# Kernel tuning notes

Hardware: AMD Instinct MI355X
Metric: run time of the kernel (lower is better)

The kernel has to match this reference:

```python
import jax, jax.numpy as jnp
import numpy as np

EPS = 1e-12  # torch F.normalize default eps (clamp_min)

def _l2norm(v, axis):
    n = jnp.sqrt(jnp.sum(v * v, axis=axis, keepdims=True))
    return v / jnp.maximum(n, EPS)

def setup_inputs() -> dict:
    key = jax.random.key(0)
    k1, k2, k3 = jax.random.split(key, 3)
    N, D, H, W, K = 64, 128, 64, 64, 32
    x = jax.random.normal(k1, (N, D, H, W), dtype=jnp.float32)
    conv_w = jax.random.normal(k2, (K, D), dtype=jnp.float32)  # 1x1 conv weight, no bias
    centroids = jax.random.uniform(k3, (K, D), dtype=jnp.float32)
    return {"x": x, "conv_w": conv_w, "centroids": centroids}

def reference(x, conv_w, centroids):
    N, D, H, W = x.shape
    K = conv_w.shape[0]
    # descriptor-wise L2 normalization over channel dim
    x = _l2norm(x, axis=1)
    xf = x.reshape(N, D, H * W)                      # [N, D, P]
    # 1x1 conv == per-pixel linear: [K,D] @ [N,D,P] -> [N,K,P]
    logits = jnp.einsum('kd,ndp->nkp', conv_w, xf)
    soft_assign = jax.nn.softmax(logits, axis=1)     # softmax over clusters
    # vlad[n,k,d] = sum_p a[n,k,p]*(x[n,d,p] - c[k,d])
    #            = (a @ x^T)[n,k,d] - (sum_p a)[n,k] * c[k,d]
    agg = jnp.einsum('nkp,ndp->nkd', soft_assign, xf)
    asum = jnp.sum(soft_assign, axis=2)              # [N, K]
    vlad = agg - asum[:, :, None] * centroids[None]  # [N, K, D]
    vlad = _l2norm(vlad, axis=2)                     # intra-normalization
    vlad = vlad.reshape(N, K * D)
    vlad = _l2norm(vlad, axis=1)                     # global L2 norm
    return vlad
```

## Files before the change

kernel.cpp:

```cpp
#include <hip/hip_runtime.h>
#include <math.h>

#define N_IMG 64
#define D_CH  128
#define P_PIX 4096
#define K_CL  32
#define S_SPL 8
#define P_BLK (P_PIX / S_SPL)
#define TP    32
#define N_TILE (P_BLK / TP)

typedef __attribute__((ext_vector_type(8))) short bf16x8;
typedef __attribute__((ext_vector_type(4))) float f32x4;

#define MFMA(a, b, c) __builtin_amdgcn_mfma_f32_16x16x32_bf16(a, b, c, 0, 0, 0)

#define BAR() do {                                            \
    asm volatile("s_waitcnt lgkmcnt(0)" ::: "memory");        \
    __builtin_amdgcn_s_barrier();                             \
} while (0)

static __device__ __forceinline__ ushort f2bf_rne(float f) {
    unsigned u = __float_as_uint(f);
    unsigned r = u + 0x7fffu + ((u >> 16) & 1u);
    return (ushort)(r >> 16);
}
static __device__ __forceinline__ ushort4 rne4(float a, float b, float c, float d) {
    ushort4 h;
    h.x = f2bf_rne(a); h.y = f2bf_rne(b); h.z = f2bf_rne(c); h.w = f2bf_rne(d);
    return h;
}

static __device__ __forceinline__ void split4t(float a, float b, float c, float d,
                                               ushort4 &h, ushort4 &l) {
    unsigned ua = __float_as_uint(a), ub = __float_as_uint(b);
    unsigned uc = __float_as_uint(c), ud = __float_as_uint(d);
    h.x = (ushort)(ua >> 16); h.y = (ushort)(ub >> 16);
    h.z = (ushort)(uc >> 16); h.w = (ushort)(ud >> 16);
    float ra = a - __uint_as_float(ua & 0xffff0000u);
    float rb = b - __uint_as_float(ub & 0xffff0000u);
    float rc = c - __uint_as_float(uc & 0xffff0000u);
    float rd = d - __uint_as_float(ud & 0xffff0000u);
    l.x = (ushort)(__float_as_uint(ra) >> 16);
    l.y = (ushort)(__float_as_uint(rb) >> 16);
    l.z = (ushort)(__float_as_uint(rc) >> 16);
    l.w = (ushort)(__float_as_uint(rd) >> 16);
}

#define STAGE_AND_PREFETCH(tt) do {                                          \
    const int cc_ = (tt) & 1;                                                \
    _Pragma("unroll")                                                        \
    for (int it = 0; it < 4; ++it) {                                         \
        int d_ = it * 32 + (tid >> 3);                                       \
        *(ushort4*)&xDh[cc_][d_ * 40 + 4 * (tid & 7)] =                      \
            rne4(xv[it].x, xv[it].y, xv[it].z, xv[it].w);                    \
    }                                                                        \
    float sq_ = 0.f;                                                         \
    _Pragma("unroll")                                                        \
    for (int c_ = 0; c_ < 4; ++c_) {                                         \
        *(ushort4*)&xTh[pT * 136 + dbase + 4 * c_] =                         \
            rne4(tv[4*c_+0], tv[4*c_+1], tv[4*c_+2], tv[4*c_+3]);            \
        sq_ += tv[4*c_+0]*tv[4*c_+0] + tv[4*c_+1]*tv[4*c_+1]                 \
             + tv[4*c_+2]*tv[4*c_+2] + tv[4*c_+3]*tv[4*c_+3];                \
    }                                                                        \
    sq_ += __shfl_xor(sq_, 32);                                              \
    if (l < 32) pbuf[wid][pT] = sq_;                                         \
    if ((tt) + 1 < N_TILE) {                                                 \
        const float* xt2_ = xin + ((tt) + 1) * TP;                           \
        _Pragma("unroll")                                                    \
        for (int it = 0; it < 4; ++it) {                                     \
            int d_ = it * 32 + (tid >> 3);                                   \
            xv[it] = *(const float4*)(xt2_ + d_ * P_PIX + 4 * (tid & 7));    \
        }                                                                    \
        _Pragma("unroll")                                                    \
        for (int j_ = 0; j_ < 16; ++j_)                                      \
            tv[j_] = xt2_[(size_t)(dbase + j_) * P_PIX + pT];                \
    }                                                                        \
} while (0)

__global__ __launch_bounds__(256)
void netvlad_main(const float* __restrict__ x, const float* __restrict__ w,
                  float* __restrict__ aggp, float* __restrict__ asump)
{
    __shared__ __align__(16) ushort xTh[32 * 136];
    __shared__ __align__(16) ushort xDh[2][128 * 40];
    __shared__ __align__(16) ushort aph[2][32 * 40];
    __shared__ __align__(16) float  xch[4][64][4];
    __shared__ float pbuf[4][32];
    __shared__ float asw[4][16];

    const int tid = threadIdx.x;
    const int n   = blockIdx.x >> 3;
    const int ps  = blockIdx.x & 7;

    const int l   = tid & 63;
    const int wid = tid >> 6;
    const int q   = l >> 4;
    const int ln  = l & 15;
    const int mt  = wid >> 1;
    const int nt  = wid & 1;

    bf16x8 wh[4], wl[4];
    #pragma unroll
    for (int kk = 0; kk < 4; ++kk) {
        const float* wp = w + (nt * 16 + ln) * D_CH + kk * 32 + 8 * q;
        float4 wa = *(const float4*)wp;
        float4 wb = *(const float4*)(wp + 4);
        ushort4 h1, l1, h2, l2;
        split4t(wa.x, wa.y, wa.z, wa.w, h1, l1);
        split4t(wb.x, wb.y, wb.z, wb.w, h2, l2);
        wh[kk][0] = (short)h1.x; wh[kk][1] = (short)h1.y; wh[kk][2] = (short)h1.z; wh[kk][3] = (short)h1.w;
        wh[kk][4] = (short)h2.x; wh[kk][5] = (short)h2.y; wh[kk][6] = (short)h2.z; wh[kk][7] = (short)h2.w;
        wl[kk][0] = (short)l1.x; wl[kk][1] = (short)l1.y; wl[kk][2] = (short)l1.z; wl[kk][3] = (short)l1.w;
        wl[kk][4] = (short)l2.x; wl[kk][5] = (short)l2.y; wl[kk][6] = (short)l2.z; wl[kk][7] = (short)l2.w;
    }

    f32x4 acc2[2][2];
    #pragma unroll
    for (int a = 0; a < 2; ++a)
        #pragma unroll
        for (int b = 0; b < 2; ++b)
            acc2[a][b] = (f32x4){0.f, 0.f, 0.f, 0.f};
    float asacc = 0.0f;

    const float* xin = x + (size_t)n * D_CH * P_PIX + ps * P_BLK;

    const int pT    = tid & 31;
    const int dbase = (tid >> 5) * 16;

    float4 xv[4];
    float  tv[16];
    {
        const float* xt = xin;
        #pragma unroll
        for (int it = 0; it < 4; ++it) {
            int d = it * 32 + (tid >> 3);
            xv[it] = *(const float4*)(xt + d * P_PIX + 4 * (tid & 7));
        }
        #pragma unroll
        for (int j = 0; j < 16; ++j)
            tv[j] = xt[(size_t)(dbase + j) * P_PIX + pT];
    }
    STAGE_AND_PREFETCH(0);

    for (int t = 0; t < N_TILE; ++t) {
        const int c = t & 1;
        BAR();

        float spx, spy, spz, spw;
        {
            int pp = l & 31;
            int jb = (l >> 5) * 2;
            float vsq = pbuf[jb][pp] + pbuf[jb + 1][pp];
            vsq += __shfl_xor(vsq, 32);
            float sSl = 1.0f / fmaxf(sqrtf(vsq), 1e-12f);
            int p0 = mt * 16 + 4 * q;
            spx = __shfl(sSl, p0 + 0);
            spy = __shfl(sSl, p0 + 1);
            spz = __shfl(sSl, p0 + 2);
            spw = __shfl(sSl, p0 + 3);
        }

        f32x4 acc1 = (f32x4){0.f, 0.f, 0.f, 0.f};
        #pragma unroll
        for (int kk = 0; kk < 4; ++kk) {
            int ia = (mt * 16 + ln) * 136 + kk * 32 + 8 * q;
            bf16x8 Ah = *(const bf16x8*)&xTh[ia];
            acc1 = MFMA(Ah, wh[kk], acc1);
            acc1 = MFMA(Ah, wl[kk], acc1);
        }

        float e[4], s[4];
        e[0] = __builtin_expf(acc1[0] * spx);
        e[1] = __builtin_expf(acc1[1] * spy);
        e[2] = __builtin_expf(acc1[2] * spz);
        e[3] = __builtin_expf(acc1[3] * spw);
        #pragma unroll
        for (int r = 0; r < 4; ++r) {
            s[r] = e[r];
            s[r] += __shfl_xor(s[r], 1);
            s[r] += __shfl_xor(s[r], 2);
            s[r] += __shfl_xor(s[r], 4);
            s[r] += __shfl_xor(s[r], 8);
        }
        *(float4*)&xch[wid][l][0] = make_float4(s[0], s[1], s[2], s[3]);
        BAR();
        {
            float4 po = *(const float4*)&xch[wid ^ 1][l][0];
            float rt[4];
            rt[0] = __builtin_amdgcn_rcpf(s[0] + po.x);
            rt[1] = __builtin_amdgcn_rcpf(s[1] + po.y);
            rt[2] = __builtin_amdgcn_rcpf(s[2] + po.z);
            rt[3] = __builtin_amdgcn_rcpf(s[3] + po.w);
            float sm[4];
            #pragma unroll
            for (int r = 0; r < 4; ++r) sm[r] = e[r] * rt[r];
            asacc += sm[0] + sm[1] + sm[2] + sm[3];
            int ib = (nt * 16 + ln) * 40 + mt * 16 + 4 * q;
            *(ushort4*)&aph[c][ib] =
                rne4(sm[0] * spx, sm[1] * spy, sm[2] * spz, sm[3] * spw);
        }
        BAR();

        bf16x8 A2h[2], B2h[2];
        #pragma unroll
        for (int m2 = 0; m2 < 2; ++m2) {
            int ia = ((2 * wid + m2) * 16 + ln) * 40 + 8 * q;
            A2h[m2] = *(const bf16x8*)&xDh[c][ia];
        }
        #pragma unroll
        for (int n2 = 0; n2 < 2; ++n2) {
            int ib = (n2 * 16 + ln) * 40 + 8 * q;
            B2h[n2] = *(const bf16x8*)&aph[c][ib];
        }
        #pragma unroll
        for (int m2 = 0; m2 < 2; ++m2)
            #pragma unroll
            for (int n2 = 0; n2 < 2; ++n2)
                acc2[m2][n2] = MFMA(A2h[m2], B2h[n2], acc2[m2][n2]);
        if (t + 1 < N_TILE) {
            STAGE_AND_PREFETCH(t + 1);
        }
    }

    const int base = ((n * S_SPL + ps) * K_CL) * D_CH;
    #pragma unroll
    for (int m2 = 0; m2 < 2; ++m2)
        #pragma unroll
        for (int n2 = 0; n2 < 2; ++n2) {
            int k = n2 * 16 + ln;
            #pragma unroll
            for (int r = 0; r < 4; ++r) {
                int d = (2 * wid + m2) * 16 + 4 * q + r;
                aggp[base + k * D_CH + d] = acc2[m2][n2][r];
            }
        }
    asacc += __shfl_xor(asacc, 16);
    asacc += __shfl_xor(asacc, 32);
    if (l < 16) asw[wid][l] = asacc;
    __syncthreads();
    if (tid < K_CL)
        asump[(n * S_SPL + ps) * K_CL + tid] =
            asw[tid >> 4][tid & 15] + asw[(tid >> 4) + 2][tid & 15];
}

__global__ __launch_bounds__(256)
void netvlad_finish(const float* __restrict__ aggp, const float* __restrict__ asump,
                    const float* __restrict__ cen, float* __restrict__ out)
{
    __shared__ float red[K_CL][8];
    __shared__ float gw[4];
    __shared__ float gss;
    const int tid = threadIdx.x;
    const int n = blockIdx.x;
    const int k = tid >> 3;
    const int d0 = (tid & 7) << 4;

    float v[16];
    #pragma unroll
    for (int i = 0; i < 16; ++i) v[i] = 0.0f;
    float as = 0.0f;
    for (int qq = 0; qq < S_SPL; ++qq) {
        const float* src = aggp + (((n * S_SPL + qq) * K_CL) + k) * D_CH + d0;
        #pragma unroll
        for (int c = 0; c < 4; ++c) {
            float4 t4 = *(const float4*)(src + (c << 2));
            v[4*c+0] += t4.x; v[4*c+1] += t4.y; v[4*c+2] += t4.z; v[4*c+3] += t4.w;
        }
        as += asump[(n * S_SPL + qq) * K_CL + k];
    }
    const float* cp = cen + k * D_CH + d0;
    float ssq = 0.0f;
    #pragma unroll
    for (int c = 0; c < 4; ++c) {
        float4 c4 = *(const float4*)(cp + (c << 2));
        v[4*c+0] -= as * c4.x;
        v[4*c+1] -= as * c4.y;
        v[4*c+2] -= as * c4.z;
        v[4*c+3] -= as * c4.w;
    }
    #pragma unroll
    for (int i = 0; i < 16; ++i) ssq += v[i] * v[i];
    red[k][tid & 7] = ssq;
    __syncthreads();
    float s2 = 0.0f;
    #pragma unroll
    for (int j = 0; j < 8; ++j) s2 += red[k][j];
    const float sc1 = 1.0f / fmaxf(sqrtf(s2), 1e-12f);
    #pragma unroll
    for (int i = 0; i < 16; ++i) v[i] *= sc1;
    float g = ssq * sc1 * sc1;
    #pragma unroll
    for (int off = 1; off < 64; off <<= 1) g += __shfl_xor(g, off);
    if ((tid & 63) == 0) gw[tid >> 6] = g;
    __syncthreads();
    if (tid == 0) gss = 1.0f / fmaxf(sqrtf(gw[0] + gw[1] + gw[2] + gw[3]), 1e-12f);
    __syncthreads();
    const float gsc = gss;
    float* op = out + (size_t)n * (K_CL * D_CH) + k * D_CH + d0;
    #pragma unroll
    for (int c = 0; c < 4; ++c) {
        *(float4*)(op + (c << 2)) =
            make_float4(v[4*c+0]*gsc, v[4*c+1]*gsc, v[4*c+2]*gsc, v[4*c+3]*gsc);
    }
}

extern "C" void kernel_launch(void* const* d_in, const int* in_sizes, int n_in,
                              void* d_out, int out_size, void* d_ws, size_t ws_size,
                              hipStream_t stream)
{
    const float* x   = (const float*)d_in[0];
    const float* w   = (const float*)d_in[1];
    const float* cen = (const float*)d_in[2];
    float* out = (float*)d_out;

    float* aggp  = (float*)d_ws;
    float* asump = aggp + (size_t)N_IMG * S_SPL * K_CL * D_CH;

    netvlad_main<<<N_IMG * S_SPL, 256, 0, stream>>>(x, w, aggp, asump);
    netvlad_finish<<<N_IMG, 256, 0, stream>>>(aggp, asump, cen, out);
}
```

Measured before the change: 46.82 us.

## Double pixel tile to 64 per iteration to halve barriers and loop trips

Raises the per-iteration pixel tile from 32 to 64. Each iteration now processes two 32-pixel halves in the logits and aggregation MFMAs, and the shared-memory buffers and their strides are resized to match. This halves the number of loop trips and barrier rounds per block and puts more loads in flight per prefetch. The cost is larger register arrays (32 transposed loads and 8 float4 per thread) and more LDS, which may reduce occupancy or cause spills.

```diff
diff --git a/kernel.cpp b/kernel.cpp
--- a/kernel.cpp
+++ b/kernel.cpp
@@ -7,8 +7,11 @@
 #define K_CL  32
 #define S_SPL 8
 #define P_BLK (P_PIX / S_SPL)
-#define TP    32
+#define TP    64
 #define N_TILE (P_BLK / TP)
+#define XDS   72
+#define APS   72
+#define XTS   136
 
 typedef __attribute__((ext_vector_type(8))) short bf16x8;
 typedef __attribute__((ext_vector_type(4))) float f32x4;
@@ -50,30 +53,29 @@
 #define STAGE_AND_PREFETCH(tt) do {                                          \
     const int cc_ = (tt) & 1;                                                \
     _Pragma("unroll")                                                        \
-    for (int it = 0; it < 4; ++it) {                                         \
-        int d_ = it * 32 + (tid >> 3);                                       \
-        *(ushort4*)&xDh[cc_][d_ * 40 + 4 * (tid & 7)] =                      \
+    for (int it = 0; it < 8; ++it) {                                         \
+        int d_ = it * 16 + (tid >> 4);                                       \
+        *(ushort4*)&xDh[cc_][d_ * XDS + 4 * (tid & 15)] =                    \
             rne4(xv[it].x, xv[it].y, xv[it].z, xv[it].w);                    \
     }                                                                        \
     float sq_ = 0.f;                                                         \
     _Pragma("unroll")                                                        \
-    for (int c_ = 0; c_ < 4; ++c_) {                                         \
-        *(ushort4*)&xTh[pT * 136 + dbase + 4 * c_] =                         \
+    for (int c_ = 0; c_ < 8; ++c_) {                                         \
+        *(ushort4*)&xTh[pT * XTS + dbase + 4 * c_] =                         \
             rne4(tv[4*c_+0], tv[4*c_+1], tv[4*c_+2], tv[4*c_+3]);            \
         sq_ += tv[4*c_+0]*tv[4*c_+0] + tv[4*c_+1]*tv[4*c_+1]                 \
              + tv[4*c_+2]*tv[4*c_+2] + tv[4*c_+3]*tv[4*c_+3];                \
     }                                                                        \
-    sq_ += __shfl_xor(sq_, 32);                                              \
-    if (l < 32) pbuf[wid][pT] = sq_;                                         \
+    pbuf[wid][pT] = sq_;                                                     \
     if ((tt) + 1 < N_TILE) {                                                 \
         const float* xt2_ = xin + ((tt) + 1) * TP;                           \
         _Pragma("unroll")                                                    \
-        for (int it = 0; it < 4; ++it) {                                     \
-            int d_ = it * 32 + (tid >> 3);                                   \
-            xv[it] = *(const float4*)(xt2_ + d_ * P_PIX + 4 * (tid & 7));    \
+        for (int it = 0; it < 8; ++it) {                                     \
+            int d_ = it * 16 + (tid >> 4);                                   \
+            xv[it] = *(const float4*)(xt2_ + (size_t)d_ * P_PIX + 4 * (tid & 15)); \
         }                                                                    \
         _Pragma("unroll")                                                    \
-        for (int j_ = 0; j_ < 16; ++j_)                                      \
+        for (int j_ = 0; j_ < 32; ++j_)                                      \
             tv[j_] = xt2_[(size_t)(dbase + j_) * P_PIX + pT];                \
     }                                                                        \
 } while (0)
@@ -82,11 +84,11 @@
 void netvlad_main(const float* __restrict__ x, const float* __restrict__ w,
                   float* __restrict__ aggp, float* __restrict__ asump)
 {
-    __shared__ __align__(16) ushort xTh[32 * 136];
-    __shared__ __align__(16) ushort xDh[2][128 * 40];
-    __shared__ __align__(16) ushort aph[2][32 * 40];
-    __shared__ __align__(16) float  xch[4][64][4];
-    __shared__ float pbuf[4][32];
+    __shared__ __align__(16) ushort xTh[64 * XTS];
+    __shared__ __align__(16) ushort xDh[2][128 * XDS];
+    __shared__ __align__(16) ushort aph[2][32 * APS];
+    __shared__ __align__(16) float  xch[4][64][8];
+    __shared__ float pbuf[4][64];
     __shared__ float asw[4][16];
 
     const int tid = threadIdx.x;
@@ -125,20 +127,20 @@
 
     const float* xin = x + (size_t)n * D_CH * P_PIX + ps * P_BLK;
 
-    const int pT    = tid & 31;
-    const int dbase = (tid >> 5) * 16;
-
-    float4 xv[4];
-    float  tv[16];
+    const int pT    = l;
+    const int dbase = wid * 32;
+
+    float4 xv[8];
+    float  tv[32];
     {
         const float* xt = xin;
         #pragma unroll
-        for (int it = 0; it < 4; ++it) {
-            int d = it * 32 + (tid >> 3);
-            xv[it] = *(const float4*)(xt + d * P_PIX + 4 * (tid & 7));
-        }
-        #pragma unroll
-        for (int j = 0; j < 16; ++j)
+        for (int it = 0; it < 8; ++it) {
+            int d = it * 16 + (tid >> 4);
+            xv[it] = *(const float4*)(xt + (size_t)d * P_PIX + 4 * (tid & 15));
+        }
+        #pragma unroll
+        for (int j = 0; j < 32; ++j)
             tv[j] = xt[(size_t)(dbase + j) * P_PIX + pT];
     }
     STAGE_AND_PREFETCH(0);
@@ -147,77 +149,83 @@
         const int c = t & 1;
         BAR();
 
-        float spx, spy, spz, spw;
+        float sp[2][4];
         {
-            int pp = l & 31;
-            int jb = (l >> 5) * 2;
-            float vsq = pbuf[jb][pp] + pbuf[jb + 1][pp];
-            vsq += __shfl_xor(vsq, 32);
+            float vsq = pbuf[0][l] + pbuf[1][l] + pbuf[2][l] + pbuf[3][l];
             float sSl = 1.0f / fmaxf(sqrtf(vsq), 1e-12f);
-            int p0 = mt * 16 + 4 * q;
-            spx = __shfl(sSl, p0 + 0);
-            spy = __shfl(sSl, p0 + 1);
-            spz = __shfl(sSl, p0 + 2);
-            spw = __shfl(sSl, p0 + 3);
-        }
-
-        f32x4 acc1 = (f32x4){0.f, 0.f, 0.f, 0.f};
-        #pragma unroll
-        for (int kk = 0; kk < 4; ++kk) {
-            int ia = (mt * 16 + ln) * 136 + kk * 32 + 8 * q;
-            bf16x8 Ah = *(const bf16x8*)&xTh[ia];
-            acc1 = MFMA(Ah, wh[kk], acc1);
-            acc1 = MFMA(Ah, wl[kk], acc1);
-        }
-
-        float e[4], s[4];
-        e[0] = __builtin_expf(acc1[0] * spx);
-        e[1] = __builtin_expf(acc1[1] * spy);
-        e[2] = __builtin_expf(acc1[2] * spz);
-        e[3] = __builtin_expf(acc1[3] * spw);
-        #pragma unroll
-        for (int r = 0; r < 4; ++r) {
-            s[r] = e[r];
-            s[r] += __shfl_xor(s[r], 1);
-            s[r] += __shfl_xor(s[r], 2);
-            s[r] += __shfl_xor(s[r], 4);
-            s[r] += __shfl_xor(s[r], 8);
-        }
-        *(float4*)&xch[wid][l][0] = make_float4(s[0], s[1], s[2], s[3]);
+            #pragma unroll
+            for (int ph = 0; ph < 2; ++ph)
+                #pragma unroll
+                for (int r = 0; r < 4; ++r)
+                    sp[ph][r] = __shfl(sSl, ph * 32 + mt * 16 + 4 * q + r);
+        }
+
+        f32x4 acc1[2];
+        #pragma unroll
+        for (int ph = 0; ph < 2; ++ph) {
+            acc1[ph] = (f32x4){0.f, 0.f, 0.f, 0.f};
+            #pragma unroll
+            for (int kk = 0; kk < 4; ++kk) {
+                int ia = (ph * 32 + mt * 16 + ln) * XTS + kk * 32 + 8 * q;
+                bf16x8 Ah = *(const bf16x8*)&xTh[ia];
+                acc1[ph] = MFMA(Ah, wh[kk], acc1[ph]);
+                acc1[ph] = MFMA(Ah, wl[kk], acc1[ph]);
+            }
+        }
+
+        float e[2][4], s[2][4];
+        #pragma unroll
+        for (int ph = 0; ph < 2; ++ph) {
+            #pragma unroll
+            for (int r = 0; r < 4; ++r) {
+                e[ph][r] = __builtin_expf(acc1[ph][r] * sp[ph][r]);
+                s[ph][r] = e[ph][r];
+                s[ph][r] += __shfl_xor(s[ph][r], 1);
+                s[ph][r] += __shfl_xor(s[ph][r], 2);
+                s[ph][r] += __shfl_xor(s[ph][r], 4);
+                s[ph][r] += __shfl_xor(s[ph][r], 8);
+            }
+        }
+        *(float4*)&xch[wid][l][0] = make_float4(s[0][0], s[0][1], s[0][2], s[0][3]);
+        *(float4*)&xch[wid][l][4] = make_float4(s[1][0], s[1][1], s[1][2], s[1][3]);
         BAR();
-        {
-            float4 po = *(const float4*)&xch[wid ^ 1][l][0];
+        #pragma unroll
+        for (int ph = 0; ph < 2; ++ph) {
+            float4 po = *(const float4*)&xch[wid ^ 1][l][ph * 4];
             float rt[4];
-            rt[0] = __builtin_amdgcn_rcpf(s[0] + po.x);
-            rt[1] = __builtin_amdgcn_rcpf(s[1] + po.y);
-            rt[2] = __builtin_amdgcn_rcpf(s[2] + po.z);
-            rt[3] = __builtin_amdgcn_rcpf(s[3] + po.w);
+            rt[0] = __builtin_amdgcn_rcpf(s[ph][0] + po.x);
+            rt[1] = __builtin_amdgcn_rcpf(s[ph][1] + po.y);
+            rt[2] = __builtin_amdgcn_rcpf(s[ph][2] + po.z);
+            rt[3] = __builtin_amdgcn_rcpf(s[ph][3] + po.w);
             float sm[4];
             #pragma unroll
-            for (int r = 0; r < 4; ++r) sm[r] = e[r] * rt[r];
+            for (int r = 0; r < 4; ++r) sm[r] = e[ph][r] * rt[r];
             asacc += sm[0] + sm[1] + sm[2] + sm[3];
-            int ib = (nt * 16 + ln) * 40 + mt * 16 + 4 * q;
-            *(ushort4*)&aph[c][ib] =
-                rne4(sm[0] * spx, sm[1] * spy, sm[2] * spz, sm[3] * spw);
+            int ib = (nt * 16 + ln) * APS + ph * 32 + mt * 16 + 4 * q;
+            *(ushort4*)&aph[c][ib] = rne4(sm[0] * sp[ph][0], sm[1] * sp[ph][1],
+                                          sm[2] * sp[ph][2], sm[3] * sp[ph][3]);
         }
         BAR();
 
-        bf16x8 A2h[2], B2h[2];
-        #pragma unroll
-        for (int m2 = 0; m2 < 2; ++m2) {
-            int ia = ((2 * wid + m2) * 16 + ln) * 40 + 8 * q;
-            A2h[m2] = *(const bf16x8*)&xDh[c][ia];
-        }
-        #pragma unroll
-        for (int n2 = 0; n2 < 2; ++n2) {
-            int ib = (n2 * 16 + ln) * 40 + 8 * q;
-            B2h[n2] = *(const bf16x8*)&aph[c][ib];
-        }
-        #pragma unroll
-        for (int m2 = 0; m2 < 2; ++m2)
-            #pragma unroll
-            for (int n2 = 0; n2 < 2; ++n2)
-                acc2[m2][n2] = MFMA(A2h[m2], B2h[n2], acc2[m2][n2]);
+        #pragma unroll
+        for (int pc = 0; pc < 2; ++pc) {
+            bf16x8 A2h[2], B2h[2];
+            #pragma unroll
+            for (int m2 = 0; m2 < 2; ++m2) {
+                int ia = ((2 * wid + m2) * 16 + ln) * XDS + pc * 32 + 8 * q;
+                A2h[m2] = *(const bf16x8*)&xDh[c][ia];
+            }
+            #pragma unroll
+            for (int n2 = 0; n2 < 2; ++n2) {
+                int ib = (n2 * 16 + ln) * APS + pc * 32 + 8 * q;
+                B2h[n2] = *(const bf16x8*)&aph[c][ib];
+            }
+            #pragma unroll
+            for (int m2 = 0; m2 < 2; ++m2)
+                #pragma unroll
+                for (int n2 = 0; n2 < 2; ++n2)
+                    acc2[m2][n2] = MFMA(A2h[m2], B2h[n2], acc2[m2][n2]);
+        }
         if (t + 1 < N_TILE) {
             STAGE_AND_PREFETCH(t + 1);
         }
```

Result: faster. 45.41 us (median of 2 runs) (-3.0%).
